# Performance work log

Hardware: AMD Instinct MI355X
Metric: run time of the kernel (lower is better)

## Reference

```python
import jax, jax.numpy as jnp
import numpy as np
import math

B, S, H = 8, 1024, 1024
LN_EPS = 1e-5  # assumed epsilon of create_normalization_layer('layer_norm')


def setup_inputs() -> dict:
    key = jax.random.key(0)
    ks = jax.random.split(key, 6)
    context = jax.random.normal(ks[0], (B, S, H), dtype=jnp.float32)
    mask = jnp.ones((B, 1, S), dtype=jnp.int32)
    prior = jax.random.uniform(ks[1], (B, S, S), dtype=jnp.float32)
    # LayerNorm params
    gamma = jnp.ones((H,), dtype=jnp.float32)
    beta = jnp.zeros((H,), dtype=jnp.float32)
    # Dense projections (Glorot-like init)
    scale = 1.0 / np.sqrt(H)
    Wk = jax.random.normal(ks[2], (H, H), dtype=jnp.float32) * scale
    bk = jnp.zeros((H,), dtype=jnp.float32)
    Wq = jax.random.normal(ks[3], (H, H), dtype=jnp.float32) * scale
    bq = jnp.zeros((H,), dtype=jnp.float32)
    return {"context": context, "mask": mask, "prior": prior,
            "gamma": gamma, "beta": beta, "Wk": Wk, "bk": bk, "Wq": Wq, "bq": bq}


def reference(context, mask, prior, gamma, beta, Wk, bk, Wq, bq):
    dtype = context.dtype
    s = context.shape[1]
    hs = context.shape[2]
    i = jnp.arange(s)
    adj_upper = i[:, None] == (i[None, :] - 1)          # [S,S] superdiagonal
    adj_lower = i[:, None] == (i[None, :] + 1)          # subdiagonal
    adj_mask = adj_upper | adj_lower
    pad = mask[:, 0, :].astype(bool)                    # [B,S]
    pad2d = pad[:, :, None] & pad[:, None, :]           # [B,S,S]
    final_adj = adj_mask[None, :, :] & pad2d

    # LayerNorm over last axis
    mu = jnp.mean(context, axis=-1, keepdims=True)
    var = jnp.mean(jnp.square(context - mu), axis=-1, keepdims=True)
    cn = (context - mu) * jax.lax.rsqrt(var + LN_EPS) * gamma + beta

    k = cn @ Wk + bk                                    # [B,S,H]
    q = cn @ Wq + bq
    scores = jnp.einsum('bsh,bth->bst', q, k) / math.sqrt(hs)
    scores = jnp.where(final_adj, scores, jnp.asarray(-1e9, dtype))
    neibor = jax.nn.softmax(scores, axis=-1)
    neibor = jnp.sqrt(neibor * jnp.swapaxes(neibor, 1, 2) + 1e-9)
    neibor = prior + (1.0 - prior) * neibor

    triu = i[None, :] >= i[:, None]                     # [S,S] upper incl diag
    tri = triu.astype(dtype)
    b_eye = jnp.eye(s, dtype=bool)

    t = jnp.log(neibor + 1e-9)
    t = jnp.where(adj_upper[None, :, :], t, jnp.asarray(0.0, dtype))
    t = jnp.einsum('bij,jk->bik', t, tri)               # cumulative over cols
    g = jnp.exp(jnp.einsum('ij,bjk->bik', tri, t))      # hierarchical prefix product
    keep = jnp.logical_not(jnp.logical_xor(triu, b_eye))
    g = jnp.where(keep[None, :, :], g, jnp.asarray(0.0, dtype))
    neibor_diag = jnp.where(b_eye[None, :, :], jnp.asarray(1e-9, dtype), neibor)
    g = g + jnp.swapaxes(g, 1, 2) + neibor_diag
    g = g / (jnp.sum(g, axis=-1, keepdims=True) + 1e-9)

    f2d = pad2d.astype(dtype)
    g = g * f2d
    neibor = neibor * f2d
    return g, neibor
```

## Files before the change

kernel.cpp:

```cpp
#include <hip/hip_runtime.h>
#include <hip/hip_bf16.h>

#define SB 8
#define SS 1024
#define SH 1024
#define LN_EPS 1e-5f

typedef unsigned short u16;
typedef __attribute__((ext_vector_type(8))) short bf16x8;
typedef __attribute__((ext_vector_type(4))) float f32x4;

__device__ __forceinline__ u16 f2bf(float f) {
  __hip_bfloat16 h = __float2bfloat16(f);
  return *reinterpret_cast<u16*>(&h);
}
__device__ __forceinline__ float bf2f(u16 x) {
  unsigned v = ((unsigned)x) << 16;
  return __builtin_bit_cast(float, v);
}

__device__ __forceinline__ void gld16(const void* g, void* l) {
  __builtin_amdgcn_global_load_lds(
      (const __attribute__((address_space(1))) void*)g,
      (__attribute__((address_space(3))) void*)l, 16, 0, 0);
}

__global__ __launch_bounds__(256) void prep(const float* __restrict__ x,
                                            const float* __restrict__ gamma,
                                            const float* __restrict__ beta,
                                            const float* __restrict__ Wq,
                                            const float* __restrict__ Wk,
                                            const float* __restrict__ bq,
                                            u16* __restrict__ cnb,
                                            u16* __restrict__ Wq_bf,
                                            u16* __restrict__ Wk_bf,
                                            float* __restrict__ wkbq,
                                            float* __restrict__ du,
                                            float* __restrict__ dd) {
  __shared__ float p1[4], p2[4];
  const int blk = blockIdx.x;
  const int t = threadIdx.x;
  const int wave = t >> 6, lane = t & 63;

  if (blk < SB * SS) {
    const float* xr = x + (size_t)blk * SH;
    float4 v = *(const float4*)(xr + 4 * t);

    float s = v.x + v.y + v.z + v.w;
#pragma unroll
    for (int off = 32; off > 0; off >>= 1) s += __shfl_down(s, off, 64);
    if (lane == 0) p1[wave] = s;
    __syncthreads();
    const float mu = (p1[0] + p1[1] + p1[2] + p1[3]) * (1.0f / SH);

    float d0 = v.x - mu, d1 = v.y - mu, d2 = v.z - mu, d3 = v.w - mu;
    float ss = d0 * d0 + d1 * d1 + d2 * d2 + d3 * d3;
#pragma unroll
    for (int off = 32; off > 0; off >>= 1) ss += __shfl_down(ss, off, 64);
    if (lane == 0) p2[wave] = ss;
    __syncthreads();
    const float rstd =
        rsqrtf((p2[0] + p2[1] + p2[2] + p2[3]) * (1.0f / SH) + LN_EPS);

    float4 gm = *(const float4*)(gamma + 4 * t);
    float4 bt = *(const float4*)(beta + 4 * t);
    ushort4 o;
    o.x = f2bf(d0 * rstd * gm.x + bt.x);
    o.y = f2bf(d1 * rstd * gm.y + bt.y);
    o.z = f2bf(d2 * rstd * gm.z + bt.z);
    o.w = f2bf(d3 * rstd * gm.w + bt.w);
    *(ushort4*)(cnb + (size_t)blk * SH + 4 * t) = o;
    if (t == 0) {
      du[blk] = 0.f;
      dd[blk] = 0.f;
    }
  } else {
    const int w = blk - SB * SS;
    const bool is_q = (w < SH);
    const float* src = is_q ? (Wq + (size_t)w * SH) : (Wk + (size_t)(w - SH) * SH);
    u16* dst = is_q ? (Wq_bf + (size_t)w * SH) : (Wk_bf + (size_t)(w - SH) * SH);
    float4 v = *(const float4*)(src + 4 * t);
    ushort4 o;
    o.x = f2bf(v.x); o.y = f2bf(v.y); o.z = f2bf(v.z); o.w = f2bf(v.w);
    *(ushort4*)(dst + 4 * t) = o;
    if (!is_q) {
      float4 b = *(const float4*)(bq + 4 * t);
      float s = v.x * b.x + v.y * b.y + v.z * b.z + v.w * b.w;
#pragma unroll
      for (int off = 32; off > 0; off >>= 1) s += __shfl_down(s, off, 64);
      if (lane == 0) p1[wave] = s;
      __syncthreads();
      if (t == 0) wkbq[w - SH] = p1[0] + p1[1] + p1[2] + p1[3];
    }
  }
}

#define GK 1024
#define GN 1024

__global__ __launch_bounds__(256) void gemm_pt64(const u16* __restrict__ A,
                                                 const u16* __restrict__ Bt,
                                                 u16* __restrict__ C) {
  __shared__ u16 As[64 * 32];
  __shared__ u16 Bs[64 * 32];
  const int tid = threadIdx.x;
  const int m0 = blockIdx.y * 64;
  const int n0 = blockIdx.x * 64;
  const int wave = tid >> 6, lane = tid & 63;
  const int wn = wave * 16;
  const int l15 = lane & 15, q = lane >> 4;

  f32x4 acc[4] = {};

  const int srow = tid >> 2;
  const int scol = 8 * (tid & 3);
  const u16* gA = A + (size_t)(m0 + srow) * GK + scol;
  const u16* gB = Bt + (size_t)(n0 + srow) * GK + scol;
  u16* lA = &As[srow * 32 + scol];
  u16* lB = &Bs[srow * 32 + scol];

  for (int k0 = 0; k0 < GK; k0 += 32) {
    __syncthreads();
    gld16(gA + k0, lA);
    gld16(gB + k0, lB);
    __syncthreads();

    bf16x8 af[4];
#pragma unroll
    for (int fm = 0; fm < 4; ++fm)
      af[fm] = *(const bf16x8*)&As[(fm * 16 + l15) * 32 + q * 8];
    bf16x8 bfr = *(const bf16x8*)&Bs[(wn + l15) * 32 + q * 8];
#pragma unroll
    for (int fm = 0; fm < 4; ++fm)
      acc[fm] = __builtin_amdgcn_mfma_f32_16x16x32_bf16(af[fm], bfr, acc[fm],
                                                        0, 0, 0);
  }

#pragma unroll
  for (int fm = 0; fm < 4; ++fm) {
    const int row0 = m0 + fm * 16 + q * 4;
    const int col = n0 + wn + l15;
#pragma unroll
    for (int r = 0; r < 4; ++r)
      C[(size_t)(row0 + r) * GN + col] = f2bf(acc[fm][r]);
  }
}

#define BM 128
#define BN 128
#define BK 32
#define KSPLIT 512

__global__ __launch_bounds__(256) void ugemm_fused(const u16* __restrict__ A,
                                                   const u16* __restrict__ Bt,
                                                   const u16* __restrict__ cnb,
                                                   const float* __restrict__ wkbq,
                                                   float* __restrict__ du,
                                                   float* __restrict__ dd) {
  __shared__ u16 As[BM * BK];
  __shared__ u16 Bs[BN * BK];
  const int tid = threadIdx.x;
  const int m0 = blockIdx.y * BM;
  const int n0 = blockIdx.x * BN;
  const int kbase = blockIdx.z * KSPLIT;
  const int wave = tid >> 6, lane = tid & 63;
  const int wm = (wave & 1) * 64, wn = (wave >> 1) * 64;
  const int l15 = lane & 15, q = lane >> 4;

  f32x4 acc[4][4] = {};

  const int srow = tid >> 2;
  const int scol = 8 * (tid & 3);
  const u16* gA = A + (size_t)(m0 + srow) * GK + kbase + scol;
  const u16* gB = Bt + (size_t)(n0 + srow) * GK + kbase + scol;
  u16* lA = &As[srow * BK + scol];
  u16* lB = &Bs[srow * BK + scol];

  for (int k0 = 0; k0 < KSPLIT; k0 += BK) {
    __syncthreads();
    gld16(gA + k0, lA);
    gld16(gA + (size_t)64 * GK + k0, lA + 64 * BK);
    gld16(gB + k0, lB);
    gld16(gB + (size_t)64 * GK + k0, lB + 64 * BK);
    __syncthreads();

    bf16x8 af[4], bfr[4];
#pragma unroll
    for (int fm = 0; fm < 4; ++fm)
      af[fm] = *(const bf16x8*)&As[(wm + fm * 16 + l15) * BK + q * 8];
#pragma unroll
    for (int fn = 0; fn < 4; ++fn)
      bfr[fn] = *(const bf16x8*)&Bs[(wn + fn * 16 + l15) * BK + q * 8];
#pragma unroll
    for (int fm = 0; fm < 4; ++fm)
#pragma unroll
      for (int fn = 0; fn < 4; ++fn)
        acc[fm][fn] = __builtin_amdgcn_mfma_f32_16x16x32_bf16(
            af[fm], bfr[fn], acc[fm][fn], 0, 0, 0);
  }

  float wb[4];
  const float wgate = (blockIdx.z == 0) ? 1.f : 0.f;
#pragma unroll
  for (int fn = 0; fn < 4; ++fn)
    wb[fn] = wgate * wkbq[n0 + wn + fn * 16 + l15];

#pragma unroll
  for (int fm = 0; fm < 4; ++fm) {
#pragma unroll
    for (int rr = 0; rr < 4; ++rr) {
      const int r = m0 + wm + fm * 16 + q * 4 + rr;
      const int sl = r & (SS - 1);
      float sdu = 0.f, sdd = 0.f;
#pragma unroll
      for (int fn = 0; fn < 4; ++fn) {
        const int col = n0 + wn + fn * 16 + l15;
        const float a = acc[fm][fn][rr] + wb[fn];
        if (sl < SS - 1) sdu += a * bf2f(cnb[(size_t)(r + 1) * SH + col]);
        if (sl > 0)      sdd += a * bf2f(cnb[(size_t)(r - 1) * SH + col]);
      }
#pragma unroll
      for (int m = 1; m < 16; m <<= 1) {
        sdu += __shfl_xor(sdu, m, 64);
        sdd += __shfl_xor(sdd, m, 64);
      }
      if (l15 == 0) {
        atomicAdd(&du[r], sdu);
        atomicAdd(&dd[r], sdd);
      }
    }
  }
}

__device__ __forceinline__ void soft2(const float* __restrict__ du,
                                      const float* __restrict__ dd, int x,
                                      float& pu, float& pd) {
  const int sl = x & (SS - 1);
  if (sl == 0) { pu = 1.f; pd = 0.f; }
  else if (sl == SS - 1) { pu = 0.f; pd = 1.f; }
  else {
    const float a = du[x] * 0.03125f;
    const float b = dd[x] * 0.03125f;
    const float m = fmaxf(a, b);
    const float eu = __expf(a - m), ed = __expf(b - m);
    const float inv = 1.f / (eu + ed);
    pu = eu * inv;
    pd = ed * inv;
  }
}

__global__ __launch_bounds__(256) void rows_fused(const float* __restrict__ prior,
                                                  const int* __restrict__ mask,
                                                  const float* __restrict__ du,
                                                  const float* __restrict__ dd,
                                                  float* __restrict__ g_out,
                                                  float* __restrict__ ne_out) {
  const int r = blockIdx.x;
  const int b = r >> 10, i = r & (SS - 1);
  const int t = threadIdx.x;
  const int wave = t >> 6, lane = t & 63;
  const float nbz = 3.1622776601683795e-5f;

  float nb_im1 = nbz, nb_ip1 = nbz;
  if (i >= 1) {
    float pu_m, pd_m, pu_c, pd_c;
    soft2(du, dd, r - 1, pu_m, pd_m);
    soft2(du, dd, r, pu_c, pd_c);
    nb_im1 = sqrtf(pu_m * pd_c + 1e-9f);
  }
  if (i <= SS - 2) {
    float pu_c, pd_c, pu_p, pd_p;
    soft2(du, dd, r, pu_c, pd_c);
    soft2(du, dd, r + 1, pu_p, pd_p);
    nb_ip1 = sqrtf(pu_c * pd_p + 1e-9f);
  }

  const float* prow = prior + (size_t)r * SS;
  float4 pr = *(const float4*)(prow + 4 * t);
  const int* mrow = mask + b * SS;
  const float padi = (mrow[i] != 0) ? 1.f : 0.f;
  int4 mk = *(const int4*)(mrow + 4 * t);

  float ne[4], gsum = 0.f;
#pragma unroll
  for (int v = 0; v < 4; ++v) {
    const int k = 4 * t + v;
    const float p = (&pr.x)[v];
    const float nb = (k == i - 1) ? nb_im1 : (k == i + 1) ? nb_ip1 : nbz;
    const float n = p + (1.f - p) * nb;
    ne[v] = n;
    gsum += (k == i) ? (2.f + 1e-9f) : (1.f + n);
  }

  __shared__ float part[4];
#pragma unroll
  for (int off = 32; off > 0; off >>= 1) gsum += __shfl_down(gsum, off, 64);
  if (lane == 0) part[wave] = gsum;
  __syncthreads();
  const float inv = 1.f / (part[0] + part[1] + part[2] + part[3] + 1e-9f);

  float4 go, no;
#pragma unroll
  for (int v = 0; v < 4; ++v) {
    const int k = 4 * t + v;
    const float padk = ((&mk.x)[v] != 0) ? 1.f : 0.f;
    const float f2 = padi * padk;
    const float gt = (k == i) ? (2.f + 1e-9f) : (1.f + ne[v]);
    (&go.x)[v] = gt * inv * f2;
    (&no.x)[v] = ne[v] * f2;
  }
  *(float4*)(g_out + (size_t)r * SS + 4 * t) = go;
  *(float4*)(ne_out + (size_t)r * SS + 4 * t) = no;
}

extern "C" void kernel_launch(void* const* d_in, const int* in_sizes, int n_in,
                              void* d_out, int out_size, void* d_ws, size_t ws_size,
                              hipStream_t stream) {
  const float* context = (const float*)d_in[0];
  const int* mask = (const int*)d_in[1];
  const float* prior = (const float*)d_in[2];
  const float* gamma = (const float*)d_in[3];
  const float* beta = (const float*)d_in[4];
  const float* Wk = (const float*)d_in[5];
  const float* bk = (const float*)d_in[6];
  const float* Wq = (const float*)d_in[7];
  const float* bq = (const float*)d_in[8];
  (void)bk;

  float* out_g = (float*)d_out;
  float* out_n = out_g + (size_t)SB * SS * SS;

  char* ws = (char*)d_ws;
  u16* cnb = (u16*)ws;
  u16* Wq_bf = (u16*)(ws + ((size_t)16 << 20));
  u16* Wk_bf = (u16*)(ws + ((size_t)18 << 20));
  u16* PT = (u16*)(ws + ((size_t)20 << 20));
  float* wkbq = (float*)(ws + ((size_t)22 << 20));
  float* du = (float*)(ws + ((size_t)23 << 20));
  float* dd = (float*)(ws + ((size_t)24 << 20));

  prep<<<SB * SS + 2 * SH, 256, 0, stream>>>(context, gamma, beta, Wq, Wk, bq,
                                             cnb, Wq_bf, Wk_bf, wkbq, du, dd);
  gemm_pt64<<<dim3(16, 16), 256, 0, stream>>>(Wk_bf, Wq_bf, PT);
  ugemm_fused<<<dim3(8, 64, 2), 256, 0, stream>>>(cnb, PT, cnb, wkbq, du, dd);
  rows_fused<<<SB * SS, 256, 0, stream>>>(prior, mask, du, dd, out_g, out_n);
}
```

Measured before the change: 205.3 us.

## Drop split-K in fused GEMM and stage neighbor rows in LDS for epilogue

The fused GEMM no longer splits K across two z-blocks; each block now walks the full K dimension, which halves the atomic adds into du/dd and drops the bias gating. The epilogue first loads the 130 neighboring rows of cn for the tile into shared memory with vector loads. It then reads the up and down neighbors from LDS instead of issuing scattered global bf16 loads. The trade-offs are a grid half as large (512 blocks), which lowers parallelism, and about 34KB of extra LDS per block, which may reduce occupancy.

```diff
diff --git a/kernel.cpp b/kernel.cpp
--- a/kernel.cpp
+++ b/kernel.cpp
@@ -149,7 +149,7 @@
 #define BM 128
 #define BN 128
 #define BK 32
-#define KSPLIT 512
+#define CNP 132
 
 __global__ __launch_bounds__(256) void ugemm_fused(const u16* __restrict__ A,
                                                    const u16* __restrict__ Bt,
@@ -159,10 +159,10 @@
                                                    float* __restrict__ dd) {
   __shared__ u16 As[BM * BK];
   __shared__ u16 Bs[BN * BK];
+  __shared__ u16 cn_s[130 * CNP];
   const int tid = threadIdx.x;
   const int m0 = blockIdx.y * BM;
   const int n0 = blockIdx.x * BN;
-  const int kbase = blockIdx.z * KSPLIT;
   const int wave = tid >> 6, lane = tid & 63;
   const int wm = (wave & 1) * 64, wn = (wave >> 1) * 64;
   const int l15 = lane & 15, q = lane >> 4;
@@ -171,12 +171,12 @@
 
   const int srow = tid >> 2;
   const int scol = 8 * (tid & 3);
-  const u16* gA = A + (size_t)(m0 + srow) * GK + kbase + scol;
-  const u16* gB = Bt + (size_t)(n0 + srow) * GK + kbase + scol;
+  const u16* gA = A + (size_t)(m0 + srow) * GK + scol;
+  const u16* gB = Bt + (size_t)(n0 + srow) * GK + scol;
   u16* lA = &As[srow * BK + scol];
   u16* lB = &Bs[srow * BK + scol];
 
-  for (int k0 = 0; k0 < KSPLIT; k0 += BK) {
+  for (int k0 = 0; k0 < GK; k0 += BK) {
     __syncthreads();
     gld16(gA + k0, lA);
     gld16(gA + (size_t)64 * GK + k0, lA + 64 * BK);
@@ -199,26 +199,40 @@
             af[fm], bfr[fn], acc[fm][fn], 0, 0, 0);
   }
 
+  {
+    const int c4 = (tid & 31) * 4;
+    for (int rowi = (tid >> 5); rowi < 130; rowi += 8) {
+      int gr = m0 - 1 + rowi;
+      gr = max(0, min(SB * SS - 1, gr));
+      *(ushort4*)&cn_s[rowi * CNP + c4] =
+          *(const ushort4*)&cnb[(size_t)gr * SH + n0 + c4];
+    }
+  }
+  __syncthreads();
+
   float wb[4];
-  const float wgate = (blockIdx.z == 0) ? 1.f : 0.f;
-#pragma unroll
-  for (int fn = 0; fn < 4; ++fn)
-    wb[fn] = wgate * wkbq[n0 + wn + fn * 16 + l15];
+#pragma unroll
+  for (int fn = 0; fn < 4; ++fn) wb[fn] = wkbq[n0 + wn + fn * 16 + l15];
 
 #pragma unroll
   for (int fm = 0; fm < 4; ++fm) {
 #pragma unroll
     for (int rr = 0; rr < 4; ++rr) {
-      const int r = m0 + wm + fm * 16 + q * 4 + rr;
+      const int lr = wm + fm * 16 + q * 4 + rr;
+      const int r = m0 + lr;
       const int sl = r & (SS - 1);
+      const u16* up = &cn_s[(lr + 2) * CNP + wn];
+      const u16* dn = &cn_s[lr * CNP + wn];
       float sdu = 0.f, sdd = 0.f;
 #pragma unroll
       for (int fn = 0; fn < 4; ++fn) {
-        const int col = n0 + wn + fn * 16 + l15;
+        const int lc = fn * 16 + l15;
         const float a = acc[fm][fn][rr] + wb[fn];
-        if (sl < SS - 1) sdu += a * bf2f(cnb[(size_t)(r + 1) * SH + col]);
-        if (sl > 0)      sdd += a * bf2f(cnb[(size_t)(r - 1) * SH + col]);
+        sdu += a * bf2f(up[lc]);
+        sdd += a * bf2f(dn[lc]);
       }
+      if (sl == SS - 1) sdu = 0.f;
+      if (sl == 0) sdd = 0.f;
 #pragma unroll
       for (int m = 1; m < 16; m <<= 1) {
         sdu += __shfl_xor(sdu, m, 64);
@@ -342,6 +356,6 @@
   prep<<<SB * SS + 2 * SH, 256, 0, stream>>>(context, gamma, beta, Wq, Wk, bq,
                                              cnb, Wq_bf, Wk_bf, wkbq, du, dd);
   gemm_pt64<<<dim3(16, 16), 256, 0, stream>>>(Wk_bf, Wq_bf, PT);
-  ugemm_fused<<<dim3(8, 64, 2), 256, 0, stream>>>(cnb, PT, cnb, wkbq, du, dd);
+  ugemm_fused<<<dim3(8, 64), 256, 0, stream>>>(cnb, PT, cnb, wkbq, du, dd);
   rows_fused<<<SB * SS, 256, 0, stream>>>(prior, mask, du, dd, out_g, out_n);
 }
```

Result: faster. 190.6 us (-7.2%).
